# Kernel optimization log

Hardware: AMD Instinct MI355X
Metric: run time of the kernel (lower is better)

The kernel has to match this reference:

```python
import jax, jax.numpy as jnp
import numpy as np

GN_GROUPS = 32
GN_EPS = 1e-6


def setup_inputs() -> dict:
    key = jax.random.key(0)
    ks = jax.random.split(key, 4)
    B, C, H, W = 8, 512, 32, 32
    x = jax.random.normal(ks[0], (B, C, H, W), dtype=jnp.float32)
    W_qkv = jax.random.normal(ks[1], (C, 3 * C), dtype=jnp.float32) * 0.02
    b_qkv = jnp.zeros((3 * C,), dtype=jnp.float32)
    W_out = jax.random.normal(ks[2], (C, C), dtype=jnp.float32) * 0.02
    b_out = jnp.zeros((C,), dtype=jnp.float32)
    gn_scale = jnp.ones((C,), dtype=jnp.float32)
    gn_bias = jnp.zeros((C,), dtype=jnp.float32)
    return {"x": x, "gn_scale": gn_scale, "gn_bias": gn_bias,
            "W_qkv": W_qkv, "b_qkv": b_qkv, "W_out": W_out, "b_out": b_out,
            "num_heads": 8}


def _group_norm(x, scale, bias):
    B, C, H, W = x.shape
    g = GN_GROUPS
    xg = x.reshape(B, g, C // g, H * W)
    mean = xg.mean(axis=(2, 3), keepdims=True)
    var = xg.var(axis=(2, 3), keepdims=True)
    xg = (xg - mean) * jax.lax.rsqrt(var + GN_EPS)
    x = xg.reshape(B, C, H, W)
    return x * scale[None, :, None, None] + bias[None, :, None, None]


def reference(x, gn_scale, gn_bias, W_qkv, b_qkv, W_out, b_out, num_heads):
    B, C, H, W = x.shape
    hd = C // num_heads
    h = _group_norm(x, gn_scale, gn_bias)
    # NIN: 1x1 projection over channels -> (B, 3C, H, W)
    h = jnp.einsum('bchw,cd->bdhw', h, W_qkv) + b_qkv[None, :, None, None]
    # reshape exactly like torch: (B, nh, 3*hd, HW) then move seq last->middle
    h = h.reshape(B, num_heads, 3 * hd, H * W).transpose(0, 1, 3, 2)  # (B, nh, S, 3hd)
    q, k, v = jnp.split(h, 3, axis=-1)  # each (B, nh, S, hd)
    scale = 1.0 / jnp.sqrt(jnp.asarray(hd, dtype=q.dtype))
    logits = jnp.einsum('bhsd,bhtd->bhst', q, k) * scale  # (B, nh, S, S)
    attn = jax.nn.softmax(logits, axis=-1)
    vals = jnp.einsum('bhst,bhtd->bhsd', attn, v)  # (B, nh, S, hd)
    h = vals.transpose(0, 1, 3, 2).reshape(B, C, H, W)
    h = jnp.einsum('bchw,cd->bdhw', h, W_out) + b_out[None, :, None, None]
    return x + h
```

## Files before the change

kernel.cpp:

```cpp
#include <hip/hip_runtime.h>
#include <hip/hip_bf16.h>

typedef __bf16 bf16_t;
typedef __attribute__((ext_vector_type(8))) __bf16 bf16x8;
typedef __attribute__((ext_vector_type(4))) float f32x4;
typedef __attribute__((ext_vector_type(4))) unsigned int u32x4;

#define B_   8
#define C_   512
#define S_   1024
#define NH   8
#define C2_  1024
#define C3_  1536
#define QSCALE 0.1803368801111204f

static __device__ __forceinline__ unsigned pack2(float a, float b) {
  unsigned short lo = __builtin_bit_cast(unsigned short, (bf16_t)a);
  unsigned short hi = __builtin_bit_cast(unsigned short, (bf16_t)b);
  return (unsigned)lo | ((unsigned)hi << 16);
}

static __device__ __forceinline__ void load_lds16(const void* g, void* l) {
  __builtin_amdgcn_global_load_lds(
      (const __attribute__((address_space(1))) unsigned*)g,
      (__attribute__((address_space(3))) unsigned*)l, 16, 0, 0);
}

template<int ROUNDS>
static __device__ __forceinline__ void stage_swz(const bf16_t* g, int rstride,
                                                 char* lbuf, int tid) {
#pragma unroll
  for (int r = 0; r < ROUNDS; ++r) {
    int i = r * 256 + tid;
    int row = i >> 3;
    int cg = (i & 7) ^ (row & 7);
    load_lds16(g + (size_t)row * rstride + cg * 8,
               lbuf + r * 4096 + (tid & 192) * 16);
  }
}

static __device__ __forceinline__ void stage_swz512(const bf16_t* g, int rstride,
                                                    char* lbuf, int tid) {
  int row = tid >> 3;
  int cg = (tid & 7) ^ (row & 7);
  load_lds16(g + (size_t)row * rstride + cg * 8,
             lbuf + (tid & 448) * 16);
}

__global__ __launch_bounds__(256) void prep_kernel(
    const float* __restrict__ x, const float* __restrict__ gsc,
    const float* __restrict__ gbi, const float* __restrict__ Wq,
    const float* __restrict__ bq, const float* __restrict__ Wo,
    bf16_t* __restrict__ h_t, bf16_t* __restrict__ wqkvp,
    bf16_t* __restrict__ woutt, float* __restrict__ bqp) {
  __shared__ __align__(16) char smem[65568];
  int bid = blockIdx.x;
  int tid = threadIdx.x;
  if (bid < 256) {
    float* xs = (float*)smem;
    float* red = (float*)(smem + 65536);
    int b = bid >> 5, g = bid & 31;
    const f32x4* xb4 = (const f32x4*)(x + ((size_t)b * C_ + g * 16) * S_);
    float s = 0.f, s2 = 0.f;
#pragma unroll
    for (int k = 0; k < 16; ++k) {
      int vf = k * 256 + tid;
      f32x4 v = xb4[vf];
      ((f32x4*)xs)[vf] = v;
#pragma unroll
      for (int e = 0; e < 4; ++e) { s += v[e]; s2 += v[e] * v[e]; }
    }
    for (int off = 32; off > 0; off >>= 1) {
      s  += __shfl_down(s, off);
      s2 += __shfl_down(s2, off);
    }
    int wave = tid >> 6, lane = tid & 63;
    if (lane == 0) { red[wave] = s; red[4 + wave] = s2; }
    __syncthreads();
    float ts = red[0] + red[1] + red[2] + red[3];
    float t2 = red[4] + red[5] + red[6] + red[7];
    const float inv_n = 1.f / (16.f * S_);
    float mean = ts * inv_n;
    float var  = t2 * inv_n - mean * mean;
    float rstd = rsqrtf(var + 1e-6f);
    float ac[16], bc[16];
#pragma unroll
    for (int cl = 0; cl < 16; ++cl) {
      float sc = gsc[g * 16 + cl] * rstd;
      ac[cl] = sc;
      bc[cl] = gbi[g * 16 + cl] - mean * sc;
    }
#pragma unroll
    for (int k = 0; k < 4; ++k) {
      int srow = tid + k * 256;
      unsigned ow[8];
#pragma unroll
      for (int p = 0; p < 8; ++p) {
        float y0 = xs[(2 * p    ) * 1024 + srow] * ac[2 * p    ] + bc[2 * p    ];
        float y1 = xs[(2 * p + 1) * 1024 + srow] * ac[2 * p + 1] + bc[2 * p + 1];
        ow[p] = pack2(y0, y1);
      }
      bf16_t* dst = h_t + ((size_t)b * S_ + srow) * C_ + g * 16;
      u32x4 v0, v1;
#pragma unroll
      for (int e = 0; e < 4; ++e) { v0[e] = ow[e]; v1[e] = ow[4 + e]; }
      *(u32x4*)dst = v0;
      *(u32x4*)(dst + 8) = v1;
    }
  } else if (bid < 1024) {
    float* T = (float*)smem;
    int id = bid - 256;
    int d0 = (id % 48) * 32, c0 = (id / 48) * 32;
    int ld = tid & 31, lc = tid >> 5;
#pragma unroll
    for (int i = 0; i < 4; ++i) {
      int c = lc + i * 8;
      T[c * 33 + ld] = Wq[(size_t)(c0 + c) * C3_ + d0 + ld];
    }
    __syncthreads();
#pragma unroll
    for (int i = 0; i < 4; ++i) {
      int dd = lc + i * 8;
      int d = d0 + dd;
      int h = d / 192, rr = d - h * 192, part = rr >> 6, dq = rr & 63;
      float scl = (part == 0) ? QSCALE : 1.f;
      wqkvp[(size_t)(part * 512 + h * 64 + dq) * C_ + c0 + ld] =
          (bf16_t)(T[ld * 33 + dd] * scl);
    }
    if (id < 48 && tid < 32) {
      int d = d0 + tid;
      int h = d / 192, rr = d - h * 192, part = rr >> 6, dq = rr & 63;
      bqp[part * 512 + h * 64 + dq] = bq[d] * ((part == 0) ? QSCALE : 1.f);
    }
  } else {
    float* T = (float*)smem;
    int id = bid - 1024;
    int c0 = (id & 15) * 32, r0 = (id >> 4) * 32;
    int lc = tid & 31, lr = tid >> 5;
#pragma unroll
    for (int i = 0; i < 4; ++i) {
      int r = lr + i * 8;
      T[r * 33 + lc] = Wo[(size_t)(r0 + r) * C_ + c0 + lc];
    }
    __syncthreads();
#pragma unroll
    for (int i = 0; i < 4; ++i) {
      int cc = lr + i * 8;
      woutt[(size_t)(c0 + cc) * C_ + r0 + lc] = (bf16_t)T[lc * 33 + cc];
    }
  }
}

template<int MF, int NF>
static __device__ __forceinline__ void gemm_loop(
    const bf16_t* Asrc, int Astride, const bf16_t* Bsrc, int Bstride,
    char* lds, int tid, f32x4 (&acc)[MF][NF]) {
  int wave = tid >> 6, lane = tid & 63;
  int wr = wave >> 1, wc = wave & 1;
  int lr = lane & 15, lq = lane >> 4;
  char* A0 = lds;
  char* B0 = lds + MF * 4096;
  char* A1 = lds + (MF + NF) * 4096;
  char* B1 = lds + (2 * MF + NF) * 4096;
  stage_swz<MF>(Asrc, Astride, A0, tid);
  stage_swz<NF>(Bsrc, Bstride, B0, tid);
#pragma unroll 1
  for (int ks = 0; ks < 8; ++ks) {
    if (ks < 7) {
      stage_swz<MF>(Asrc + (ks + 1) * 64, Astride, (ks & 1) ? A0 : A1, tid);
      stage_swz<NF>(Bsrc + (ks + 1) * 64, Bstride, (ks & 1) ? B0 : B1, tid);
      asm volatile("s_waitcnt vmcnt(%0)" :: "i"(MF + NF) : "memory");
    } else {
      asm volatile("s_waitcnt vmcnt(0)" ::: "memory");
    }
    __builtin_amdgcn_s_barrier();
    const char* Ab = (ks & 1) ? A1 : A0;
    const char* Bb = (ks & 1) ? B1 : B0;
#pragma unroll
    for (int kk = 0; kk < 2; ++kk) {
      int co = ((kk * 4 + lq) ^ (lr & 7)) << 4;
      bf16x8 a[MF], b[NF];
#pragma unroll
      for (int i = 0; i < MF; ++i)
        a[i] = *(const bf16x8*)(Ab + (wr * MF * 16 + i * 16 + lr) * 128 + co);
#pragma unroll
      for (int j = 0; j < NF; ++j)
        b[j] = *(const bf16x8*)(Bb + (wc * NF * 16 + j * 16 + lr) * 128 + co);
#pragma unroll
      for (int i = 0; i < MF; ++i)
#pragma unroll
        for (int j = 0; j < NF; ++j)
          acc[i][j] = __builtin_amdgcn_mfma_f32_16x16x32_bf16(a[i], b[j], acc[i][j], 0, 0, 0);
    }
    __builtin_amdgcn_s_barrier();
  }
}

__global__ __launch_bounds__(256) void gemm_qkv_kernel(
    const bf16_t* __restrict__ h, const bf16_t* __restrict__ wq,
    const float* __restrict__ bias, bf16_t* __restrict__ qk,
    bf16_t* __restrict__ vt) {
  __shared__ char lds[65536];
  int tid = threadIdx.x;
  int bid = blockIdx.x;
  int wave = tid >> 6, lane = tid & 63;
  int wr = wave >> 1, wc = wave & 1, lr = lane & 15, lq = lane >> 4;
  unsigned short* tb = (unsigned short*)lds;
  if (bid < 512) {
    int m0 = (bid & 63) * 128, n0 = (bid >> 6) * 128;
    f32x4 acc[4][4] = {};
    gemm_loop<4, 4>(h + (size_t)m0 * C_, C_, wq + (size_t)n0 * C_, C_, lds, tid, acc);
    float bv[4];
#pragma unroll
    for (int j = 0; j < 4; ++j) bv[j] = bias[n0 + wc * 64 + j * 16 + lr];
#pragma unroll
    for (int i = 0; i < 4; ++i)
#pragma unroll
      for (int j = 0; j < 4; ++j)
#pragma unroll
        for (int r = 0; r < 4; ++r) {
          int row = wr * 64 + i * 16 + lq * 4 + r;
          int col = wc * 64 + j * 16 + lr;
          int byte = row * 256 + (((col >> 3) ^ (row & 7)) << 4) + ((col & 7) << 1);
          tb[byte >> 1] = __builtin_bit_cast(unsigned short, (bf16_t)(acc[i][j][r] + bv[j]));
        }
    __builtin_amdgcn_s_barrier();
#pragma unroll
    for (int u = 0; u < 8; ++u) {
      int flat = tid + u * 256;
      int row = flat >> 4, c = flat & 15;
      u32x4 v = *(const u32x4*)(lds + row * 256 + ((c ^ (row & 7)) << 4));
      int m = m0 + row, b = m >> 10, s = m & 1023;
      int d = n0 + c * 8;
      int hh = (d >> 6) & 7, det = ((d >> 9) << 6) + (d & 63);
      *(u32x4*)(qk + ((size_t)(b * S_ + s)) * C2_ + hh * 128 + det) = v;
    }
  } else {
    int j2 = bid - 512;
    int n0 = (j2 & 63) * 128, m0 = (j2 >> 6) * 128;
    f32x4 acc[4][4] = {};
    gemm_loop<4, 4>(wq + (size_t)(1024 + m0) * C_, C_, h + (size_t)n0 * C_, C_, lds, tid, acc);
    float bv[4][4];
#pragma unroll
    for (int i = 0; i < 4; ++i) {
      f32x4 t = *(const f32x4*)(bias + 1024 + m0 + wr * 64 + i * 16 + lq * 4);
#pragma unroll
      for (int r = 0; r < 4; ++r) bv[i][r] = t[r];
    }
#pragma unroll
    for (int i = 0; i < 4; ++i)
#pragma unroll
      for (int j = 0; j < 4; ++j)
#pragma unroll
        for (int r = 0; r < 4; ++r) {
          int row = wr * 64 + i * 16 + lq * 4 + r;
          int col = wc * 64 + j * 16 + lr;
          int byte = row * 256 + (((col >> 3) ^ (row & 7)) << 4) + ((col & 7) << 1);
          tb[byte >> 1] = __builtin_bit_cast(unsigned short, (bf16_t)(acc[i][j][r] + bv[i][r]));
        }
    __builtin_amdgcn_s_barrier();
#pragma unroll
    for (int u = 0; u < 8; ++u) {
      int flat = tid + u * 256;
      int row = flat >> 4, c = flat & 15;
      u32x4 v = *(const u32x4*)(lds + row * 256 + ((c ^ (row & 7)) << 4));
      int m = m0 + row;
      int hh = m >> 6, dv = m & 63;
      int n = n0 + c * 8, b = n >> 10, s = n & 1023;
      *(u32x4*)(vt + ((size_t)((b * NH + hh) * 64 + dv)) * S_ + s) = v;
    }
  }
}

__global__ __launch_bounds__(512) void attn_kernel(
    const bf16_t* __restrict__ qk, const bf16_t* __restrict__ vt,
    bf16_t* __restrict__ ao) {
  __shared__ char lds[65536];
  int bid = blockIdx.x;
  int qt = bid >> 6, g = bid & 63;
  int b = g >> 3, head = g & 7;
  int tid = threadIdx.x, wave = tid >> 6, lane = tid & 63;
  int lr = lane & 15, lq = lane >> 4;
  int qb = qt * 256 + wave * 32;
  const bf16_t* qkb = qk + (size_t)b * S_ * C2_ + head * 128;
  const bf16_t* vtb = vt + (size_t)((b * NH + head) * 64) * S_;

  bf16x8 qf[2][2];
#pragma unroll
  for (int q2 = 0; q2 < 2; ++q2)
#pragma unroll
    for (int kk = 0; kk < 2; ++kk)
      qf[q2][kk] = *(const bf16x8*)(qkb + (size_t)(qb + q2 * 16 + lr) * C2_ + kk * 32 + lq * 8);

  f32x4 oacc[2][4] = {};
  float m_run[2] = {-1e30f, -1e30f}, l_run[2] = {0.f, 0.f};

  char* s0 = lds;
  char* s1 = lds + 16384;
  char* s2 = lds + 32768;
  char* s3 = lds + 49152;

#define STAGE_KV(kt, buf)                                                    \
  do {                                                                       \
    stage_swz512(qkb + (size_t)((kt) * 64) * C2_ + 64, C2_, (buf), tid);     \
    stage_swz512(vtb + (kt) * 64, S_, (buf) + 8192, tid);                    \
  } while (0)

  STAGE_KV(0, s0);
  STAGE_KV(1, s1);
#pragma unroll 1
  for (int kt = 0; kt < 16; ++kt) {
    if (kt < 14) {
      STAGE_KV(kt + 2, s2);
      asm volatile("s_waitcnt vmcnt(4)" ::: "memory");
    } else if (kt == 14) {
      asm volatile("s_waitcnt vmcnt(2)" ::: "memory");
    } else {
      asm volatile("s_waitcnt vmcnt(0)" ::: "memory");
    }
    __builtin_amdgcn_s_barrier();

    f32x4 sacc[2][4] = {};
    __builtin_amdgcn_s_setprio(1);
#pragma unroll
    for (int kk = 0; kk < 2; ++kk) {
      int co = ((kk * 4 + lq) ^ (lr & 7)) << 4;
      bf16x8 kf[4];
#pragma unroll
      for (int mf = 0; mf < 4; ++mf)
        kf[mf] = *(const bf16x8*)(s0 + (mf * 16 + lr) * 128 + co);
#pragma unroll
      for (int q2 = 0; q2 < 2; ++q2)
#pragma unroll
        for (int mf = 0; mf < 4; ++mf)
          sacc[q2][mf] = __builtin_amdgcn_mfma_f32_16x16x32_bf16(kf[mf], qf[q2][kk], sacc[q2][mf], 0, 0, 0);
    }
    __builtin_amdgcn_s_setprio(0);

    float mx[2];
#pragma unroll
    for (int q2 = 0; q2 < 2; ++q2) {
      float m = -1e30f;
#pragma unroll
      for (int mf = 0; mf < 4; ++mf)
#pragma unroll
        for (int r = 0; r < 4; ++r) m = fmaxf(m, sacc[q2][mf][r]);
      m = fmaxf(m, __shfl_xor(m, 16));
      m = fmaxf(m, __shfl_xor(m, 32));
      mx[q2] = m;
    }
    if (__any(fmaxf(mx[0] - m_run[0], mx[1] - m_run[1]) > 11.f)) {
#pragma unroll
      for (int q2 = 0; q2 < 2; ++q2) {
        float mn = fmaxf(m_run[q2], mx[q2]);
        float alpha = __builtin_amdgcn_exp2f(m_run[q2] - mn);
        m_run[q2] = mn;
        l_run[q2] *= alpha;
#pragma unroll
        for (int df = 0; df < 4; ++df)
#pragma unroll
          for (int r = 0; r < 4; ++r) oacc[q2][df][r] *= alpha;
      }
    }
    unsigned pk[2][4][2];
#pragma unroll
    for (int q2 = 0; q2 < 2; ++q2) {
      float p[4][4];
      float rs = 0.f;
#pragma unroll
      for (int mf = 0; mf < 4; ++mf)
#pragma unroll
        for (int r = 0; r < 4; ++r) {
          float v = __builtin_amdgcn_exp2f(sacc[q2][mf][r] - m_run[q2]);
          p[mf][r] = v; rs += v;
        }
      l_run[q2] += rs;
#pragma unroll
      for (int mf = 0; mf < 4; ++mf)
#pragma unroll
        for (int j = 0; j < 2; ++j)
          pk[q2][mf][j] = pack2(p[mf][2 * j], p[mf][2 * j + 1]);
    }

#pragma unroll
    for (int kk = 0; kk < 2; ++kk) {
      int co = ((kk * 4 + lq) ^ (lr & 7)) << 4;
      bf16x8 vf[4];
#pragma unroll
      for (int df = 0; df < 4; ++df)
        vf[df] = *(const bf16x8*)(s0 + 8192 + (df * 16 + lr) * 128 + co);
#pragma unroll
      for (int q2 = 0; q2 < 2; ++q2) {
        unsigned w0 = pk[q2][2 * kk + 0][0], w2 = pk[q2][2 * kk + 1][0];
        unsigned w1 = pk[q2][2 * kk + 0][1], w3 = pk[q2][2 * kk + 1][1];
        asm("v_permlane32_swap_b32 %0, %1" : "+v"(w0), "+v"(w2));
        asm("v_permlane16_swap_b32 %0, %1" : "+v"(w0), "+v"(w2));
        asm("v_permlane32_swap_b32 %0, %1" : "+v"(w1), "+v"(w3));
        asm("v_permlane16_swap_b32 %0, %1" : "+v"(w1), "+v"(w3));
        u32x4 bw; bw[0] = w0; bw[1] = w1; bw[2] = w2; bw[3] = w3;
        bf16x8 pb = __builtin_bit_cast(bf16x8, bw);
        __builtin_amdgcn_s_setprio(1);
#pragma unroll
        for (int df = 0; df < 4; ++df)
          oacc[q2][df] = __builtin_amdgcn_mfma_f32_16x16x32_bf16(vf[df], pb, oacc[q2][df], 0, 0, 0);
        __builtin_amdgcn_s_setprio(0);
      }
    }
    char* tp = s0; s0 = s1; s1 = s2; s2 = s3; s3 = tp;
  }

#pragma unroll
  for (int q2 = 0; q2 < 2; ++q2) {
    float lt = l_run[q2];
    lt += __shfl_xor(lt, 16);
    lt += __shfl_xor(lt, 32);
    float inv = 1.f / lt;
    bf16_t* aop = ao + ((size_t)b * S_ + qb + q2 * 16 + lr) * C_ + head * 64;
#pragma unroll
    for (int df = 0; df < 4; ++df)
#pragma unroll
      for (int rp = 0; rp < 4; rp += 2) {
        unsigned u = pack2(oacc[q2][df][rp] * inv, oacc[q2][df][rp + 1] * inv);
        *(unsigned*)(aop + df * 16 + lq * 4 + rp) = u;
      }
  }
#undef STAGE_KV
}

__global__ __launch_bounds__(256) void gemm_out_kernel(
    const bf16_t* __restrict__ A, const bf16_t* __restrict__ Bw,
    const float* __restrict__ bias, const float* __restrict__ xres,
    float* __restrict__ out) {
  __shared__ char lds[49152];
  int tid = threadIdx.x;
  int bid = blockIdx.x;
  int m0 = (bid & 127) * 64, n0 = (bid >> 7) * 128;
  f32x4 acc[2][4] = {};
  gemm_loop<2, 4>(A + (size_t)m0 * C_, C_, Bw + (size_t)n0 * C_, C_, lds, tid, acc);
  int wave = tid >> 6, lane = tid & 63;
  int wr = wave >> 1, wc = wave & 1, lr = lane & 15, lq = lane >> 4;
#pragma unroll
  for (int i = 0; i < 2; ++i) {
#pragma unroll
    for (int j = 0; j < 4; ++j) {
      int d = n0 + wc * 64 + j * 16 + lr;
      int m = m0 + wr * 32 + i * 16 + lq * 4;
      int b = m >> 10, s = m & 1023;
      size_t o = ((size_t)b * C_ + d) * S_ + s;
      f32x4 res = *(const f32x4*)(xres + o);
      f32x4 val;
      float bd = bias[d];
#pragma unroll
      for (int r = 0; r < 4; ++r) val[r] = res[r] + bd + acc[i][j][r];
      *(f32x4*)(out + o) = val;
    }
  }
}

extern "C" void kernel_launch(void* const* d_in, const int* in_sizes, int n_in,
                              void* d_out, int out_size, void* d_ws, size_t ws_size,
                              hipStream_t stream) {
  const float* x        = (const float*)d_in[0];
  const float* gn_scale = (const float*)d_in[1];
  const float* gn_bias  = (const float*)d_in[2];
  const float* W_qkv    = (const float*)d_in[3];
  const float* b_qkv    = (const float*)d_in[4];
  const float* W_out    = (const float*)d_in[5];
  const float* b_out    = (const float*)d_in[6];
  float* out = (float*)d_out;

  char* ws = (char*)d_ws;
  bf16_t* h_t   = (bf16_t*)(ws);
  bf16_t* qk_t  = (bf16_t*)(ws + 8388608);
  bf16_t* vt    = (bf16_t*)(ws + 25165824);
  bf16_t* ao_t  = (bf16_t*)(ws + 33554432);
  bf16_t* wqkvp = (bf16_t*)(ws + 41943040);
  bf16_t* woutt = (bf16_t*)(ws + 43515904);
  float* bqp = (float*)d_out;

  prep_kernel<<<1280, 256, 0, stream>>>(x, gn_scale, gn_bias, W_qkv, b_qkv,
                                        W_out, h_t, wqkvp, woutt, bqp);
  gemm_qkv_kernel<<<768, 256, 0, stream>>>(h_t, wqkvp, bqp, qk_t, vt);
  attn_kernel<<<256, 512, 0, stream>>>(qk_t, vt, ao_t);
  gemm_out_kernel<<<512, 256, 0, stream>>>(ao_t, woutt, b_out, x, out);
}
```

Baseline: 75.79 us.

## Use 256x256 tiles with double-buffered async LDS staging in QKV GEMM

```diff
diff --git a/kernel.cpp b/kernel.cpp
--- a/kernel.cpp
+++ b/kernel.cpp
@@ -45,6 +45,18 @@
   int cg = (tid & 7) ^ (row & 7);
   load_lds16(g + (size_t)row * rstride + cg * 8,
              lbuf + (tid & 448) * 16);
+}
+
+static __device__ __forceinline__ void stage_tile256(const bf16_t* g,
+                                                     char* lbuf, int tid) {
+#pragma unroll
+  for (int r = 0; r < 4; ++r) {
+    int i = r * 512 + tid;
+    int row = i >> 3;
+    int cg = (i & 7) ^ (row & 7);
+    load_lds16(g + (size_t)row * C_ + cg * 8,
+               lbuf + r * 8192 + (tid & 448) * 16);
+  }
 }
 
 __global__ __launch_bounds__(256) void prep_kernel(
@@ -196,76 +208,130 @@
   }
 }
 
-__global__ __launch_bounds__(256) void gemm_qkv_kernel(
+__global__ __launch_bounds__(512, 2) void gemm_qkv_kernel(
     const bf16_t* __restrict__ h, const bf16_t* __restrict__ wq,
     const float* __restrict__ bias, bf16_t* __restrict__ qk,
     bf16_t* __restrict__ vt) {
-  __shared__ char lds[65536];
+  extern __shared__ __align__(16) char lds[];
   int tid = threadIdx.x;
   int bid = blockIdx.x;
   int wave = tid >> 6, lane = tid & 63;
-  int wr = wave >> 1, wc = wave & 1, lr = lane & 15, lq = lane >> 4;
+  int wr = wave >> 2, wc = wave & 3;
+  int lr = lane & 15, lq = lane >> 4;
+
+  bool isV = bid >= 128;
+  int m0, n0;
+  const bf16_t *Asrc, *Bsrc;
+  if (!isV) {
+    m0 = (bid & 31) * 256; n0 = (bid >> 5) * 256;
+    Asrc = h + (size_t)m0 * C_;
+    Bsrc = wq + (size_t)n0 * C_;
+  } else {
+    int j2 = bid - 128;
+    n0 = (j2 & 31) * 256; m0 = (j2 >> 5) * 256;
+    Asrc = wq + (size_t)(1024 + m0) * C_;
+    Bsrc = h + (size_t)n0 * C_;
+  }
+  char* A0 = lds;
+  char* B0 = lds + 32768;
+  char* A1 = lds + 65536;
+  char* B1 = lds + 98304;
+
+  f32x4 acc[8][4] = {};
+  stage_tile256(Asrc + 0 * 64, A0, tid);
+  stage_tile256(Bsrc + 0 * 64, B0, tid);
+  stage_tile256(Asrc + 1 * 64, A1, tid);
+  stage_tile256(Bsrc + 1 * 64, B1, tid);
+#pragma unroll 1
+  for (int kt = 0; kt < 8; ++kt) {
+    if (kt <= 6) {
+      asm volatile("s_waitcnt vmcnt(8)" ::: "memory");
+    } else {
+      asm volatile("s_waitcnt vmcnt(0)" ::: "memory");
+    }
+    __builtin_amdgcn_s_barrier();
+    char* Abuf = (kt & 1) ? A1 : A0;
+    char* Bbuf = (kt & 1) ? B1 : B0;
+#pragma unroll
+    for (int kk = 0; kk < 2; ++kk) {
+      int co = ((kk * 4 + lq) ^ (lr & 7)) << 4;
+      bf16x8 a[8], b[4];
+#pragma unroll
+      for (int i = 0; i < 8; ++i)
+        a[i] = *(const bf16x8*)(Abuf + (wr * 128 + i * 16 + lr) * 128 + co);
+#pragma unroll
+      for (int j = 0; j < 4; ++j)
+        b[j] = *(const bf16x8*)(Bbuf + (wc * 64 + j * 16 + lr) * 128 + co);
+      __builtin_amdgcn_s_setprio(1);
+#pragma unroll
+      for (int i = 0; i < 8; ++i)
+#pragma unroll
+        for (int j = 0; j < 4; ++j)
+          acc[i][j] = __builtin_amdgcn_mfma_f32_16x16x32_bf16(a[i], b[j], acc[i][j], 0, 0, 0);
+      __builtin_amdgcn_s_setprio(0);
+    }
+    __builtin_amdgcn_s_barrier();
+    if (kt < 6) {
+      stage_tile256(Asrc + (kt + 2) * 64, Abuf, tid);
+      stage_tile256(Bsrc + (kt + 2) * 64, Bbuf, tid);
+    }
+  }
+  __builtin_amdgcn_s_barrier();
+
   unsigned short* tb = (unsigned short*)lds;
-  if (bid < 512) {
-    int m0 = (bid & 63) * 128, n0 = (bid >> 6) * 128;
-    f32x4 acc[4][4] = {};
-    gemm_loop<4, 4>(h + (size_t)m0 * C_, C_, wq + (size_t)n0 * C_, C_, lds, tid, acc);
+  if (!isV) {
     float bv[4];
 #pragma unroll
     for (int j = 0; j < 4; ++j) bv[j] = bias[n0 + wc * 64 + j * 16 + lr];
 #pragma unroll
-    for (int i = 0; i < 4; ++i)
+    for (int i = 0; i < 8; ++i)
 #pragma unroll
       for (int j = 0; j < 4; ++j)
 #pragma unroll
         for (int r = 0; r < 4; ++r) {
-          int row = wr * 64 + i * 16 + lq * 4 + r;
+          int row = wr * 128 + i * 16 + lq * 4 + r;
           int col = wc * 64 + j * 16 + lr;
-          int byte = row * 256 + (((col >> 3) ^ (row & 7)) << 4) + ((col & 7) << 1);
-          tb[byte >> 1] = __builtin_bit_cast(unsigned short, (bf16_t)(acc[i][j][r] + bv[j]));
+          tb[row * 256 + col] =
+              __builtin_bit_cast(unsigned short, (bf16_t)(acc[i][j][r] + bv[j]));
         }
     __builtin_amdgcn_s_barrier();
 #pragma unroll
-    for (int u = 0; u < 8; ++u) {
-      int flat = tid + u * 256;
-      int row = flat >> 4, c = flat & 15;
-      u32x4 v = *(const u32x4*)(lds + row * 256 + ((c ^ (row & 7)) << 4));
+    for (int u = 0; u < 16; ++u) {
+      int flat = u * 512 + tid;
+      int row = flat >> 5, c = flat & 31;
+      u32x4 v = *(const u32x4*)(tb + row * 256 + c * 8);
       int m = m0 + row, b = m >> 10, s = m & 1023;
       int d = n0 + c * 8;
       int hh = (d >> 6) & 7, det = ((d >> 9) << 6) + (d & 63);
       *(u32x4*)(qk + ((size_t)(b * S_ + s)) * C2_ + hh * 128 + det) = v;
     }
   } else {
-    int j2 = bid - 512;
-    int n0 = (j2 & 63) * 128, m0 = (j2 >> 6) * 128;
-    f32x4 acc[4][4] = {};
-    gemm_loop<4, 4>(wq + (size_t)(1024 + m0) * C_, C_, h + (size_t)n0 * C_, C_, lds, tid, acc);
-    float bv[4][4];
-#pragma unroll
-    for (int i = 0; i < 4; ++i) {
-      f32x4 t = *(const f32x4*)(bias + 1024 + m0 + wr * 64 + i * 16 + lq * 4);
+    float bv[8][4];
+#pragma unroll
+    for (int i = 0; i < 8; ++i) {
+      f32x4 t = *(const f32x4*)(bias + 1024 + m0 + wr * 128 + i * 16 + lq * 4);
 #pragma unroll
       for (int r = 0; r < 4; ++r) bv[i][r] = t[r];
     }
 #pragma unroll
-    for (int i = 0; i < 4; ++i)
+    for (int i = 0; i < 8; ++i)
 #pragma unroll
       for (int j = 0; j < 4; ++j)
 #pragma unroll
         for (int r = 0; r < 4; ++r) {
-          int row = wr * 64 + i * 16 + lq * 4 + r;
+          int row = wr * 128 + i * 16 + lq * 4 + r;
           int col = wc * 64 + j * 16 + lr;
-          int byte = row * 256 + (((col >> 3) ^ (row & 7)) << 4) + ((col & 7) << 1);
-          tb[byte >> 1] = __builtin_bit_cast(unsigned short, (bf16_t)(acc[i][j][r] + bv[i][r]));
+          tb[row * 256 + col] =
+              __builtin_bit_cast(unsigned short, (bf16_t)(acc[i][j][r] + bv[i][r]));
         }
     __builtin_amdgcn_s_barrier();
 #pragma unroll
-    for (int u = 0; u < 8; ++u) {
-      int flat = tid + u * 256;
-      int row = flat >> 4, c = flat & 15;
-      u32x4 v = *(const u32x4*)(lds + row * 256 + ((c ^ (row & 7)) << 4));
-      int m = m0 + row;
-      int hh = m >> 6, dv = m & 63;
+    for (int u = 0; u < 16; ++u) {
+      int flat = u * 512 + tid;
+      int row = flat >> 5, c = flat & 31;
+      u32x4 v = *(const u32x4*)(tb + row * 256 + c * 8);
+      int dvp = m0 + row;
+      int hh = dvp >> 6, dv = dvp & 63;
       int n = n0 + c * 8, b = n >> 10, s = n & 1023;
       *(u32x4*)(vt + ((size_t)((b * NH + hh) * 64 + dv)) * S_ + s) = v;
     }
@@ -478,9 +544,12 @@
   bf16_t* woutt = (bf16_t*)(ws + 43515904);
   float* bqp = (float*)d_out;
 
+  hipFuncSetAttribute((const void*)gemm_qkv_kernel,
+                      hipFuncAttributeMaxDynamicSharedMemorySize, 131072);
+
   prep_kernel<<<1280, 256, 0, stream>>>(x, gn_scale, gn_bias, W_qkv, b_qkv,
                                         W_out, h_t, wqkvp, woutt, bqp);
-  gemm_qkv_kernel<<<768, 256, 0, stream>>>(h_t, wqkvp, bqp, qk_t, vt);
+  gemm_qkv_kernel<<<192, 512, 131072, stream>>>(h_t, wqkvp, bqp, qk_t, vt);
   attn_kernel<<<256, 512, 0, stream>>>(qk_t, vt, ao_t);
   gemm_out_kernel<<<512, 256, 0, stream>>>(ao_t, woutt, b_out, x, out);
 }
```

Measured after the change: 77.57 us. +2.3%, slower.

## Double attention KV tile to 128 keys with triple-buffered dynamic LDS

Applied to the files above, without the earlier changes.

```diff
diff --git a/kernel.cpp b/kernel.cpp
--- a/kernel.cpp
+++ b/kernel.cpp
@@ -37,14 +37,6 @@
     load_lds16(g + (size_t)row * rstride + cg * 8,
                lbuf + r * 4096 + (tid & 192) * 16);
   }
-}
-
-static __device__ __forceinline__ void stage_swz512(const bf16_t* g, int rstride,
-                                                    char* lbuf, int tid) {
-  int row = tid >> 3;
-  int cg = (tid & 7) ^ (row & 7);
-  load_lds16(g + (size_t)row * rstride + cg * 8,
-             lbuf + (tid & 448) * 16);
 }
 
 __global__ __launch_bounds__(256) void prep_kernel(
@@ -272,10 +264,10 @@
   }
 }
 
-__global__ __launch_bounds__(512) void attn_kernel(
+__global__ __launch_bounds__(512, 2) void attn_kernel(
     const bf16_t* __restrict__ qk, const bf16_t* __restrict__ vt,
     bf16_t* __restrict__ ao) {
-  __shared__ char lds[65536];
+  extern __shared__ __align__(16) char alds[];
   int bid = blockIdx.x;
   int qt = bid >> 6, g = bid & 63;
   int b = g >> 3, head = g & 7;
@@ -295,45 +287,54 @@
   f32x4 oacc[2][4] = {};
   float m_run[2] = {-1e30f, -1e30f}, l_run[2] = {0.f, 0.f};
 
-  char* s0 = lds;
-  char* s1 = lds + 16384;
-  char* s2 = lds + 32768;
-  char* s3 = lds + 49152;
+  char* s0 = alds;
+  char* s1 = alds + 32768;
+  char* s2 = alds + 65536;
 
 #define STAGE_KV(kt, buf)                                                    \
   do {                                                                       \
-    stage_swz512(qkb + (size_t)((kt) * 64) * C2_ + 64, C2_, (buf), tid);     \
-    stage_swz512(vtb + (kt) * 64, S_, (buf) + 8192, tid);                    \
+    _Pragma("unroll")                                                        \
+    for (int rr_ = 0; rr_ < 2; ++rr_) {                                      \
+      int i_ = rr_ * 512 + tid;                                              \
+      int row_ = i_ >> 3;                                                    \
+      int cg_ = (i_ & 7) ^ (row_ & 7);                                       \
+      load_lds16(qkb + (size_t)((kt) * 128 + row_) * C2_ + 64 + cg_ * 8,     \
+                 (buf) + rr_ * 8192 + (tid & 448) * 16);                     \
+    }                                                                        \
+    _Pragma("unroll")                                                        \
+    for (int rr_ = 0; rr_ < 2; ++rr_) {                                      \
+      int i_ = rr_ * 512 + tid;                                              \
+      int row_ = i_ >> 4;                                                    \
+      int cg_ = (i_ & 15) ^ (row_ & 15);                                     \
+      load_lds16(vtb + (size_t)row_ * S_ + (kt) * 128 + cg_ * 8,             \
+                 (buf) + 16384 + rr_ * 8192 + (tid & 448) * 16);             \
+    }                                                                        \
   } while (0)
 
   STAGE_KV(0, s0);
   STAGE_KV(1, s1);
 #pragma unroll 1
-  for (int kt = 0; kt < 16; ++kt) {
-    if (kt < 14) {
-      STAGE_KV(kt + 2, s2);
+  for (int kt = 0; kt < 8; ++kt) {
+    if (kt < 7) {
       asm volatile("s_waitcnt vmcnt(4)" ::: "memory");
-    } else if (kt == 14) {
-      asm volatile("s_waitcnt vmcnt(2)" ::: "memory");
     } else {
       asm volatile("s_waitcnt vmcnt(0)" ::: "memory");
     }
     __builtin_amdgcn_s_barrier();
-
-    f32x4 sacc[2][4] = {};
+    if (kt < 6) STAGE_KV(kt + 2, s2);
+
+    f32x4 sacc[2][8] = {};
     __builtin_amdgcn_s_setprio(1);
 #pragma unroll
     for (int kk = 0; kk < 2; ++kk) {
       int co = ((kk * 4 + lq) ^ (lr & 7)) << 4;
-      bf16x8 kf[4];
-#pragma unroll
-      for (int mf = 0; mf < 4; ++mf)
-        kf[mf] = *(const bf16x8*)(s0 + (mf * 16 + lr) * 128 + co);
-#pragma unroll
-      for (int q2 = 0; q2 < 2; ++q2)
-#pragma unroll
-        for (int mf = 0; mf < 4; ++mf)
-          sacc[q2][mf] = __builtin_amdgcn_mfma_f32_16x16x32_bf16(kf[mf], qf[q2][kk], sacc[q2][mf], 0, 0, 0);
+#pragma unroll
+      for (int mf = 0; mf < 8; ++mf) {
+        bf16x8 kf = *(const bf16x8*)(s0 + (mf * 16 + lr) * 128 + co);
+#pragma unroll
+        for (int q2 = 0; q2 < 2; ++q2)
+          sacc[q2][mf] = __builtin_amdgcn_mfma_f32_16x16x32_bf16(kf, qf[q2][kk], sacc[q2][mf], 0, 0, 0);
+      }
     }
     __builtin_amdgcn_s_setprio(0);
 
@@ -342,7 +343,7 @@
     for (int q2 = 0; q2 < 2; ++q2) {
       float m = -1e30f;
 #pragma unroll
-      for (int mf = 0; mf < 4; ++mf)
+      for (int mf = 0; mf < 8; ++mf)
 #pragma unroll
         for (int r = 0; r < 4; ++r) m = fmaxf(m, sacc[q2][mf][r]);
       m = fmaxf(m, __shfl_xor(m, 16));
@@ -362,37 +363,34 @@
           for (int r = 0; r < 4; ++r) oacc[q2][df][r] *= alpha;
       }
     }
-    unsigned pk[2][4][2];
+    unsigned pk[2][8][2];
 #pragma unroll
     for (int q2 = 0; q2 < 2; ++q2) {
-      float p[4][4];
       float rs = 0.f;
 #pragma unroll
-      for (int mf = 0; mf < 4; ++mf)
-#pragma unroll
-        for (int r = 0; r < 4; ++r) {
-          float v = __builtin_amdgcn_exp2f(sacc[q2][mf][r] - m_run[q2]);
-          p[mf][r] = v; rs += v;
-        }
+      for (int mf = 0; mf < 8; ++mf) {
+        float p0 = __builtin_amdgcn_exp2f(sacc[q2][mf][0] - m_run[q2]);
+        float p1 = __builtin_amdgcn_exp2f(sacc[q2][mf][1] - m_run[q2]);
+        float p2 = __builtin_amdgcn_exp2f(sacc[q2][mf][2] - m_run[q2]);
+        float p3 = __builtin_amdgcn_exp2f(sacc[q2][mf][3] - m_run[q2]);
+        rs += (p0 + p1) + (p2 + p3);
+        pk[q2][mf][0] = pack2(p0, p1);
+        pk[q2][mf][1] = pack2(p2, p3);
+      }
       l_run[q2] += rs;
-#pragma unroll
-      for (int mf = 0; mf < 4; ++mf)
-#pragma unroll
-        for (int j = 0; j < 2; ++j)
-          pk[q2][mf][j] = pack2(p[mf][2 * j], p[mf][2 * j + 1]);
-    }
-
-#pragma unroll
-    for (int kk = 0; kk < 2; ++kk) {
-      int co = ((kk * 4 + lq) ^ (lr & 7)) << 4;
+    }
+
+#pragma unroll
+    for (int kp = 0; kp < 4; ++kp) {
+      int cov = ((kp * 4 + lq) ^ lr) << 4;
       bf16x8 vf[4];
 #pragma unroll
       for (int df = 0; df < 4; ++df)
-        vf[df] = *(const bf16x8*)(s0 + 8192 + (df * 16 + lr) * 128 + co);
+        vf[df] = *(const bf16x8*)(s0 + 16384 + (df * 16 + lr) * 256 + cov);
 #pragma unroll
       for (int q2 = 0; q2 < 2; ++q2) {
-        unsigned w0 = pk[q2][2 * kk + 0][0], w2 = pk[q2][2 * kk + 1][0];
-        unsigned w1 = pk[q2][2 * kk + 0][1], w3 = pk[q2][2 * kk + 1][1];
+        unsigned w0 = pk[q2][2 * kp + 0][0], w2 = pk[q2][2 * kp + 1][0];
+        unsigned w1 = pk[q2][2 * kp + 0][1], w3 = pk[q2][2 * kp + 1][1];
         asm("v_permlane32_swap_b32 %0, %1" : "+v"(w0), "+v"(w2));
         asm("v_permlane16_swap_b32 %0, %1" : "+v"(w0), "+v"(w2));
         asm("v_permlane32_swap_b32 %0, %1" : "+v"(w1), "+v"(w3));
@@ -406,7 +404,7 @@
         __builtin_amdgcn_s_setprio(0);
       }
     }
-    char* tp = s0; s0 = s1; s1 = s2; s2 = s3; s3 = tp;
+    char* tp = s0; s0 = s1; s1 = s2; s2 = tp;
   }
 
 #pragma unroll
@@ -478,9 +476,12 @@
   bf16_t* woutt = (bf16_t*)(ws + 43515904);
   float* bqp = (float*)d_out;
 
+  hipFuncSetAttribute((const void*)attn_kernel,
+                      hipFuncAttributeMaxDynamicSharedMemorySize, 98304);
+
   prep_kernel<<<1280, 256, 0, stream>>>(x, gn_scale, gn_bias, W_qkv, b_qkv,
                                         W_out, h_t, wqkvp, woutt, bqp);
   gemm_qkv_kernel<<<768, 256, 0, stream>>>(h_t, wqkvp, bqp, qk_t, vt);
-  attn_kernel<<<256, 512, 0, stream>>>(qk_t, vt, ao_t);
+  attn_kernel<<<256, 512, 98304, stream>>>(qk_t, vt, ao_t);
   gemm_out_kernel<<<512, 256, 0, stream>>>(ao_t, woutt, b_out, x, out);
 }
```

Result: no change. 77.26 us (+1.9%).

## Software-pipeline attention: overlap previous tile's PV MFMAs with current QK

Applied to the files above, without the earlier changes.

```diff
diff --git a/kernel.cpp b/kernel.cpp
--- a/kernel.cpp
+++ b/kernel.cpp
@@ -294,32 +294,56 @@
 
   f32x4 oacc[2][4] = {};
   float m_run[2] = {-1e30f, -1e30f}, l_run[2] = {0.f, 0.f};
-
-  char* s0 = lds;
-  char* s1 = lds + 16384;
-  char* s2 = lds + 32768;
-  char* s3 = lds + 49152;
-
-#define STAGE_KV(kt, buf)                                                    \
+  unsigned pkp[2][4][2];
+
+#define STAGE_KV(kt)                                                         \
   do {                                                                       \
-    stage_swz512(qkb + (size_t)((kt) * 64) * C2_ + 64, C2_, (buf), tid);     \
-    stage_swz512(vtb + (kt) * 64, S_, (buf) + 8192, tid);                    \
+    char* buf_ = lds + (((kt) & 3) << 14);                                   \
+    stage_swz512(qkb + (size_t)((kt) * 64) * C2_ + 64, C2_, buf_, tid);      \
+    stage_swz512(vtb + (kt) * 64, S_, buf_ + 8192, tid);                     \
   } while (0)
 
-  STAGE_KV(0, s0);
-  STAGE_KV(1, s1);
+#define PV_STEP(t)                                                           \
+  do {                                                                       \
+    char* vb_ = lds + (((t) & 3) << 14) + 8192;                              \
+    _Pragma("unroll")                                                        \
+    for (int kk = 0; kk < 2; ++kk) {                                         \
+      int co_ = ((kk * 4 + lq) ^ (lr & 7)) << 4;                             \
+      bf16x8 vf_[4];                                                         \
+      _Pragma("unroll")                                                      \
+      for (int df = 0; df < 4; ++df)                                         \
+        vf_[df] = *(const bf16x8*)(vb_ + (df * 16 + lr) * 128 + co_);        \
+      _Pragma("unroll")                                                      \
+      for (int q2 = 0; q2 < 2; ++q2) {                                       \
+        unsigned w0 = pkp[q2][2 * kk + 0][0], w2 = pkp[q2][2 * kk + 1][0];   \
+        unsigned w1 = pkp[q2][2 * kk + 0][1], w3 = pkp[q2][2 * kk + 1][1];   \
+        asm("v_permlane32_swap_b32 %0, %1" : "+v"(w0), "+v"(w2));            \
+        asm("v_permlane16_swap_b32 %0, %1" : "+v"(w0), "+v"(w2));            \
+        asm("v_permlane32_swap_b32 %0, %1" : "+v"(w1), "+v"(w3));            \
+        asm("v_permlane16_swap_b32 %0, %1" : "+v"(w1), "+v"(w3));            \
+        u32x4 bw_; bw_[0] = w0; bw_[1] = w1; bw_[2] = w2; bw_[3] = w3;       \
+        bf16x8 pb_ = __builtin_bit_cast(bf16x8, bw_);                        \
+        _Pragma("unroll")                                                    \
+        for (int df = 0; df < 4; ++df)                                       \
+          oacc[q2][df] = __builtin_amdgcn_mfma_f32_16x16x32_bf16(            \
+              vf_[df], pb_, oacc[q2][df], 0, 0, 0);                          \
+      }                                                                      \
+    }                                                                        \
+  } while (0)
+
+  STAGE_KV(0);
+  STAGE_KV(1);
 #pragma unroll 1
   for (int kt = 0; kt < 16; ++kt) {
-    if (kt < 14) {
-      STAGE_KV(kt + 2, s2);
+    if (kt < 15) {
       asm volatile("s_waitcnt vmcnt(4)" ::: "memory");
-    } else if (kt == 14) {
-      asm volatile("s_waitcnt vmcnt(2)" ::: "memory");
     } else {
       asm volatile("s_waitcnt vmcnt(0)" ::: "memory");
     }
     __builtin_amdgcn_s_barrier();
-
+    if (kt < 14) STAGE_KV(kt + 2);
+
+    char* kb = lds + ((kt & 3) << 14);
     f32x4 sacc[2][4] = {};
     __builtin_amdgcn_s_setprio(1);
 #pragma unroll
@@ -328,13 +352,15 @@
       bf16x8 kf[4];
 #pragma unroll
       for (int mf = 0; mf < 4; ++mf)
-        kf[mf] = *(const bf16x8*)(s0 + (mf * 16 + lr) * 128 + co);
+        kf[mf] = *(const bf16x8*)(kb + (mf * 16 + lr) * 128 + co);
 #pragma unroll
       for (int q2 = 0; q2 < 2; ++q2)
 #pragma unroll
         for (int mf = 0; mf < 4; ++mf)
           sacc[q2][mf] = __builtin_amdgcn_mfma_f32_16x16x32_bf16(kf[mf], qf[q2][kk], sacc[q2][mf], 0, 0, 0);
     }
+
+    if (kt > 0) PV_STEP(kt - 1);
     __builtin_amdgcn_s_setprio(0);
 
     float mx[2];
@@ -362,52 +388,26 @@
           for (int r = 0; r < 4; ++r) oacc[q2][df][r] *= alpha;
       }
     }
-    unsigned pk[2][4][2];
 #pragma unroll
     for (int q2 = 0; q2 < 2; ++q2) {
-      float p[4][4];
       float rs = 0.f;
 #pragma unroll
-      for (int mf = 0; mf < 4; ++mf)
-#pragma unroll
-        for (int r = 0; r < 4; ++r) {
-          float v = __builtin_amdgcn_exp2f(sacc[q2][mf][r] - m_run[q2]);
-          p[mf][r] = v; rs += v;
-        }
+      for (int mf = 0; mf < 4; ++mf) {
+        float p0 = __builtin_amdgcn_exp2f(sacc[q2][mf][0] - m_run[q2]);
+        float p1 = __builtin_amdgcn_exp2f(sacc[q2][mf][1] - m_run[q2]);
+        float p2 = __builtin_amdgcn_exp2f(sacc[q2][mf][2] - m_run[q2]);
+        float p3 = __builtin_amdgcn_exp2f(sacc[q2][mf][3] - m_run[q2]);
+        rs += (p0 + p1) + (p2 + p3);
+        pkp[q2][mf][0] = pack2(p0, p1);
+        pkp[q2][mf][1] = pack2(p2, p3);
+      }
       l_run[q2] += rs;
-#pragma unroll
-      for (int mf = 0; mf < 4; ++mf)
-#pragma unroll
-        for (int j = 0; j < 2; ++j)
-          pk[q2][mf][j] = pack2(p[mf][2 * j], p[mf][2 * j + 1]);
-    }
-
-#pragma unroll
-    for (int kk = 0; kk < 2; ++kk) {
-      int co = ((kk * 4 + lq) ^ (lr & 7)) << 4;
-      bf16x8 vf[4];
-#pragma unroll
-      for (int df = 0; df < 4; ++df)
-        vf[df] = *(const bf16x8*)(s0 + 8192 + (df * 16 + lr) * 128 + co);
-#pragma unroll
-      for (int q2 = 0; q2 < 2; ++q2) {
-        unsigned w0 = pk[q2][2 * kk + 0][0], w2 = pk[q2][2 * kk + 1][0];
-        unsigned w1 = pk[q2][2 * kk + 0][1], w3 = pk[q2][2 * kk + 1][1];
-        asm("v_permlane32_swap_b32 %0, %1" : "+v"(w0), "+v"(w2));
-        asm("v_permlane16_swap_b32 %0, %1" : "+v"(w0), "+v"(w2));
-        asm("v_permlane32_swap_b32 %0, %1" : "+v"(w1), "+v"(w3));
-        asm("v_permlane16_swap_b32 %0, %1" : "+v"(w1), "+v"(w3));
-        u32x4 bw; bw[0] = w0; bw[1] = w1; bw[2] = w2; bw[3] = w3;
-        bf16x8 pb = __builtin_bit_cast(bf16x8, bw);
-        __builtin_amdgcn_s_setprio(1);
-#pragma unroll
-        for (int df = 0; df < 4; ++df)
-          oacc[q2][df] = __builtin_amdgcn_mfma_f32_16x16x32_bf16(vf[df], pb, oacc[q2][df], 0, 0, 0);
-        __builtin_amdgcn_s_setprio(0);
-      }
-    }
-    char* tp = s0; s0 = s1; s1 = s2; s2 = s3; s3 = tp;
-  }
+    }
+  }
+
+  __builtin_amdgcn_s_setprio(1);
+  PV_STEP(15);
+  __builtin_amdgcn_s_setprio(0);
 
 #pragma unroll
   for (int q2 = 0; q2 < 2; ++q2) {
@@ -425,6 +425,7 @@
       }
   }
 #undef STAGE_KV
+#undef PV_STEP
 }
 
 __global__ __launch_bounds__(256) void gemm_out_kernel(
```

Result: no change. 75.64 us (-0.2%).
